# Performance work log

Measured on AMD Instinct MI355X. Metric: run time of the kernel, lower is better.

Reference implementation:

```python
import jax, jax.numpy as jnp
import numpy as np

B, N, F, L = 8, 2048, 128, 2
SLOPE = 0.1  # LeakyReLU negative slope

def lrelu(v):
    return jnp.where(v >= 0, v, SLOPE * v)

def setup_inputs() -> dict:
    key = jax.random.key(0)
    ks = jax.random.split(key, 7)
    scale = 1.0 / np.sqrt(F)
    return {
        "x": jax.random.normal(ks[0], (B, N, F), dtype=jnp.float32),
        "W3": jax.random.normal(ks[1], (L, F, F), dtype=jnp.float32) * scale,
        "b3": jnp.zeros((L, F), dtype=jnp.float32),
        "W4": jax.random.normal(ks[2], (L, F, F), dtype=jnp.float32) * scale,
        "b4": jnp.zeros((L, F), dtype=jnp.float32),
        "W5": jax.random.normal(ks[3], (L, F, F), dtype=jnp.float32) * scale,
        "b5": jnp.zeros((L, F), dtype=jnp.float32),
    }

def reference(x, W3, b3, W4, b4, W5, b5):
    # GraphStack of L GraphLayer modules, mes_type '0':
    #   weight_ij = dot(LeakyReLU(g3(n_i)), LeakyReLU(g4(n_j)))
    #   message_i = mean_{j != i} weight_ij * n_j
    #   n_i_out   = LeakyReLU(g5(message_i)) + n_i
    n = x.shape[1]
    for l in range(W3.shape[0]):
        w1 = lrelu(jnp.einsum('bnf,fg->bng', x, W3[l]) + b3[l])  # [B,N,F]
        w2 = lrelu(jnp.einsum('bnf,fg->bng', x, W4[l]) + b4[l])  # [B,N,F]
        wt = jnp.einsum('bif,bjf->bij', w1, w2)                  # pairwise weights [B,N,N]
        diag = jnp.einsum('bif,bif->bi', w1, w2)                 # self weights to exclude
        msg = (jnp.einsum('bij,bjf->bif', wt, x) - diag[..., None] * x) / (n - 1)
        x = lrelu(jnp.einsum('bif,fg->big', msg, W5[l]) + b5[l]) + x
    return x
```

## Files before the change

kernel.cpp:

```cpp
#include <hip/hip_runtime.h>

#define BB 8
#define NN 2048
#define FF 128
#define NL 2
#define SLOPE 0.1f
#define NROW (BB * NN)
#define XS_STRIDE 136

typedef __attribute__((ext_vector_type(8))) short short8;
typedef __attribute__((ext_vector_type(4))) float f32x4;

__device__ __forceinline__ float lrelu(float v) { return v >= 0.f ? v : SLOPE * v; }

__device__ __forceinline__ ushort f2bf(float f) {
    uint u = __float_as_uint(f);
    return (ushort)((u + 0x7fffu + ((u >> 16) & 1u)) >> 16);
}

__global__ __launch_bounds__(256) void k_prep(
    const float* __restrict__ W3, const float* __restrict__ W4,
    const float* __restrict__ W5, ushort* __restrict__ Wt)
{
    const int idx = blockIdx.x * 256 + threadIdx.x;
    const int m = idx >> 14;
    const int rem = idx & 16383;
    const int f = rem & 127;
    const int g = rem >> 7;
    const int l = m / 3, w = m % 3;
    const float* src = (w == 0) ? W3 : (w == 1) ? W4 : W5;
    Wt[m * 16384 + g * 128 + f] = f2bf(src[l * 16384 + f * 128 + g]);
}

__global__ __launch_bounds__(256) void k_w12(
    const float* __restrict__ x, const ushort* __restrict__ w3t,
    const ushort* __restrict__ w4t, const float* __restrict__ b3,
    const float* __restrict__ b4, ushort* __restrict__ w1b,
    ushort* __restrict__ w2t, ushort* __restrict__ xt,
    float* __restrict__ diag)
{
    __shared__ ushort xs[32 * XS_STRIDE];
    __shared__ float diag_s[32];

    const int tid = threadIdx.x;
    const int row0 = blockIdx.x * 32;
    const int b = row0 >> 11;
    const int jloc0 = row0 & 2047;

    if (tid < 32) diag_s[tid] = 0.f;

    const float4* xg4 = (const float4*)(x + (size_t)row0 * FF);
#pragma unroll
    for (int i = 0; i < 4; i++) {
        const int f4 = i * 256 + tid;
        const int row = f4 >> 5;
        const int k = (f4 & 31) * 4;
        float4 v = xg4[f4];
        ushort4 h;
        h.x = f2bf(v.x); h.y = f2bf(v.y); h.z = f2bf(v.z); h.w = f2bf(v.w);
        *(ushort4*)&xs[row * XS_STRIDE + k] = h;
    }
    __syncthreads();

    {
        const int g = tid >> 1;
        const int h = tid & 1;
        uint p[8];
#pragma unroll
        for (int jj = 0; jj < 8; jj++) {
            const uint lo = xs[(h * 16 + jj * 2) * XS_STRIDE + g];
            const uint hi = xs[(h * 16 + jj * 2 + 1) * XS_STRIDE + g];
            p[jj] = lo | (hi << 16);
        }
        uint4* dst = (uint4*)&xt[(size_t)b * (FF * NN) + (size_t)g * NN + jloc0 + h * 16];
        dst[0] = make_uint4(p[0], p[1], p[2], p[3]);
        dst[1] = make_uint4(p[4], p[5], p[6], p[7]);
    }

    const int lane = tid & 63;
    const int wave = tid >> 6;
    const int c = lane & 15;
    const int quad = lane >> 4;
    const int ct0 = wave * 2;

    f32x4 acc1[2][2], acc2[2][2];
#pragma unroll
    for (int rt = 0; rt < 2; rt++)
#pragma unroll
        for (int ct = 0; ct < 2; ct++) { acc1[rt][ct] = (f32x4)0.f; acc2[rt][ct] = (f32x4)0.f; }

#pragma unroll
    for (int kk = 0; kk < 4; kk++) {
        short8 a0 = *(const short8*)&xs[c * XS_STRIDE + kk * 32 + quad * 8];
        short8 a1 = *(const short8*)&xs[(16 + c) * XS_STRIDE + kk * 32 + quad * 8];
#pragma unroll
        for (int ct = 0; ct < 2; ct++) {
            const int n = (ct0 + ct) * 16 + c;
            short8 bf3 = *(const short8*)&w3t[n * 128 + kk * 32 + quad * 8];
            short8 bf4 = *(const short8*)&w4t[n * 128 + kk * 32 + quad * 8];
            acc1[0][ct] = __builtin_amdgcn_mfma_f32_16x16x32_bf16(a0, bf3, acc1[0][ct], 0, 0, 0);
            acc1[1][ct] = __builtin_amdgcn_mfma_f32_16x16x32_bf16(a1, bf3, acc1[1][ct], 0, 0, 0);
            acc2[0][ct] = __builtin_amdgcn_mfma_f32_16x16x32_bf16(a0, bf4, acc2[0][ct], 0, 0, 0);
            acc2[1][ct] = __builtin_amdgcn_mfma_f32_16x16x32_bf16(a1, bf4, acc2[1][ct], 0, 0, 0);
        }
    }

    float dpar[2][4];
#pragma unroll
    for (int rt = 0; rt < 2; rt++)
#pragma unroll
        for (int r = 0; r < 4; r++) dpar[rt][r] = 0.f;

#pragma unroll
    for (int rt = 0; rt < 2; rt++) {
#pragma unroll
        for (int ct = 0; ct < 2; ct++) {
            const int gcol = (ct0 + ct) * 16 + c;
            const float bb3 = b3[gcol], bb4 = b4[gcol];
            ushort w2p[4];
#pragma unroll
            for (int r = 0; r < 4; r++) {
                const float v1 = lrelu(acc1[rt][ct][r] + bb3);
                const float v2 = lrelu(acc2[rt][ct][r] + bb4);
                const int grow = row0 + rt * 16 + quad * 4 + r;
                w1b[(size_t)grow * FF + gcol] = f2bf(v1);
                w2p[r] = f2bf(v2);
                dpar[rt][r] += v1 * v2;
            }
            const uint lo = (uint)w2p[0] | ((uint)w2p[1] << 16);
            const uint hi = (uint)w2p[2] | ((uint)w2p[3] << 16);
            uint2* dst = (uint2*)&w2t[(size_t)b * (FF * NN) + (size_t)gcol * NN +
                                      jloc0 + rt * 16 + quad * 4];
            *dst = make_uint2(lo, hi);
        }
    }

#pragma unroll
    for (int rt = 0; rt < 2; rt++) {
#pragma unroll
        for (int r = 0; r < 4; r++) {
            float dp = dpar[rt][r];
            dp += __shfl_xor(dp, 1, 64);
            dp += __shfl_xor(dp, 2, 64);
            dp += __shfl_xor(dp, 4, 64);
            dp += __shfl_xor(dp, 8, 64);
            if (c == 0) atomicAdd(&diag_s[rt * 16 + quad * 4 + r], dp);
        }
    }
    __syncthreads();
    if (tid < 32) diag[row0 + tid] = diag_s[tid];
}

__global__ __launch_bounds__(256) void k_S2(
    const ushort* __restrict__ xt, const ushort* __restrict__ w2t,
    ushort* __restrict__ St)
{
    __shared__ float red[4][512];
    const int tid = threadIdx.x;
    const int lane = tid & 63;
    const int wave = tid >> 6;
    const int c = lane & 15;
    const int quad = lane >> 4;

    const int b  = blockIdx.x >> 5;
    const int gq = (blockIdx.x >> 3) & 3;
    const int fs = blockIdx.x & 7;

    const ushort* xtb = xt + (size_t)b * (FF * NN);
    const ushort* w2b = w2t + (size_t)b * (FF * NN);

    const int j0 = wave * 512 + quad * 8;
    const ushort* a0p = &xtb[(gq * 32 + c) * NN + j0];
    const ushort* a1p = &xtb[(gq * 32 + 16 + c) * NN + j0];
    const ushort* bp  = &w2b[(fs * 16 + c) * NN + j0];

    f32x4 acc0 = (f32x4)0.f, acc1 = (f32x4)0.f;
#pragma unroll
    for (int it = 0; it < 16; it++) {
        short8 a0 = *(const short8*)(a0p + it * 32);
        short8 a1 = *(const short8*)(a1p + it * 32);
        short8 bf = *(const short8*)(bp + it * 32);
        acc0 = __builtin_amdgcn_mfma_f32_16x16x32_bf16(a0, bf, acc0, 0, 0, 0);
        acc1 = __builtin_amdgcn_mfma_f32_16x16x32_bf16(a1, bf, acc1, 0, 0, 0);
    }

#pragma unroll
    for (int r = 0; r < 4; r++) {
        red[wave][(quad * 4 + r) * 16 + c] = acc0[r];
        red[wave][(16 + quad * 4 + r) * 16 + c] = acc1[r];
    }
    __syncthreads();

#pragma unroll
    for (int i = 0; i < 2; i++) {
        const int idx = i * 256 + tid;
        const float s = red[0][idx] + red[1][idx] + red[2][idx] + red[3][idx];
        const int gl = idx >> 4;
        const int fl = idx & 15;
        St[(size_t)b * (FF * FF) + (size_t)(gq * 32 + gl) * FF + fs * 16 + fl] = f2bf(s);
    }
}

__global__ __launch_bounds__(256) void k_out(
    const float* __restrict__ x, const ushort* __restrict__ w1b,
    const ushort* __restrict__ St, const float* __restrict__ diag,
    const ushort* __restrict__ w5t, const float* __restrict__ b5,
    float* __restrict__ out)
{
    __shared__ ushort w1s[32 * XS_STRIDE];
    __shared__ ushort ms[32 * XS_STRIDE];

    const int tid = threadIdx.x;
    const int row0 = blockIdx.x * 32;
    const int b = row0 >> 11;
    const ushort* Sb = St + (size_t)b * (FF * FF);

#pragma unroll
    for (int i = 0; i < 2; i++) {
        const int e8 = i * 256 + tid;
        const int off = e8 * 8;
        const int row = off >> 7;
        const int k = off & 127;
        short8 v = *(const short8*)&w1b[(size_t)row0 * FF + off];
        *(short8*)&w1s[row * XS_STRIDE + k] = v;
    }
    __syncthreads();

    const int lane = tid & 63;
    const int wave = tid >> 6;
    const int c = lane & 15;
    const int quad = lane >> 4;
    const int ct0 = wave * 2;

    f32x4 accm[2][2];
#pragma unroll
    for (int rt = 0; rt < 2; rt++)
#pragma unroll
        for (int ct = 0; ct < 2; ct++) accm[rt][ct] = (f32x4)0.f;

#pragma unroll
    for (int kk = 0; kk < 4; kk++) {
        short8 a0 = *(const short8*)&w1s[c * XS_STRIDE + kk * 32 + quad * 8];
        short8 a1 = *(const short8*)&w1s[(16 + c) * XS_STRIDE + kk * 32 + quad * 8];
#pragma unroll
        for (int ct = 0; ct < 2; ct++) {
            const int n = (ct0 + ct) * 16 + c;
            short8 bf = *(const short8*)&Sb[n * 128 + kk * 32 + quad * 8];
            accm[0][ct] = __builtin_amdgcn_mfma_f32_16x16x32_bf16(a0, bf, accm[0][ct], 0, 0, 0);
            accm[1][ct] = __builtin_amdgcn_mfma_f32_16x16x32_bf16(a1, bf, accm[1][ct], 0, 0, 0);
        }
    }

    const float inv = 1.f / (float)(NN - 1);
    float xsv[2][2][4];
#pragma unroll
    for (int rt = 0; rt < 2; rt++) {
        float dg[4];
#pragma unroll
        for (int r = 0; r < 4; r++) dg[r] = diag[row0 + rt * 16 + quad * 4 + r];
#pragma unroll
        for (int ct = 0; ct < 2; ct++) {
            const int gcol = (ct0 + ct) * 16 + c;
#pragma unroll
            for (int r = 0; r < 4; r++) {
                const int lrow = rt * 16 + quad * 4 + r;
                const float xv = x[(size_t)(row0 + lrow) * FF + gcol];
                xsv[rt][ct][r] = xv;
                const float m = (accm[rt][ct][r] - dg[r] * xv) * inv;
                ms[lrow * XS_STRIDE + gcol] = f2bf(m);
            }
        }
    }
    __syncthreads();

    f32x4 acc2[2][2];
#pragma unroll
    for (int rt = 0; rt < 2; rt++)
#pragma unroll
        for (int ct = 0; ct < 2; ct++) acc2[rt][ct] = (f32x4)0.f;

#pragma unroll
    for (int kk = 0; kk < 4; kk++) {
        short8 a0 = *(const short8*)&ms[c * XS_STRIDE + kk * 32 + quad * 8];
        short8 a1 = *(const short8*)&ms[(16 + c) * XS_STRIDE + kk * 32 + quad * 8];
#pragma unroll
        for (int ct = 0; ct < 2; ct++) {
            const int n = (ct0 + ct) * 16 + c;
            short8 bf = *(const short8*)&w5t[n * 128 + kk * 32 + quad * 8];
            acc2[0][ct] = __builtin_amdgcn_mfma_f32_16x16x32_bf16(a0, bf, acc2[0][ct], 0, 0, 0);
            acc2[1][ct] = __builtin_amdgcn_mfma_f32_16x16x32_bf16(a1, bf, acc2[1][ct], 0, 0, 0);
        }
    }

#pragma unroll
    for (int rt = 0; rt < 2; rt++) {
#pragma unroll
        for (int ct = 0; ct < 2; ct++) {
            const int gcol = (ct0 + ct) * 16 + c;
            const float bb = b5[gcol];
#pragma unroll
            for (int r = 0; r < 4; r++) {
                const int grow = row0 + rt * 16 + quad * 4 + r;
                out[(size_t)grow * FF + gcol] = lrelu(acc2[rt][ct][r] + bb) + xsv[rt][ct][r];
            }
        }
    }
}

__global__ __launch_bounds__(256) void k_out_w12(
    const float* __restrict__ x, const ushort* __restrict__ w1b_in,
    const ushort* __restrict__ St, const float* __restrict__ diag_in,
    const ushort* __restrict__ w5t, const float* __restrict__ b5,
    float* __restrict__ out,
    const ushort* __restrict__ w3t, const ushort* __restrict__ w4t,
    const float* __restrict__ b3, const float* __restrict__ b4,
    ushort* __restrict__ w1b, ushort* __restrict__ w2t,
    ushort* __restrict__ xt, float* __restrict__ diag)
{
    __shared__ ushort sA[32 * XS_STRIDE];
    __shared__ ushort sB[32 * XS_STRIDE];
    __shared__ float diag_s[32];

    const int tid = threadIdx.x;
    const int row0 = blockIdx.x * 32;
    const int b = row0 >> 11;
    const int jloc0 = row0 & 2047;
    const ushort* Sb = St + (size_t)b * (FF * FF);

    if (tid < 32) diag_s[tid] = 0.f;

#pragma unroll
    for (int i = 0; i < 2; i++) {
        const int e8 = i * 256 + tid;
        const int off = e8 * 8;
        const int row = off >> 7;
        const int k = off & 127;
        short8 v = *(const short8*)&w1b_in[(size_t)row0 * FF + off];
        *(short8*)&sA[row * XS_STRIDE + k] = v;
    }
    __syncthreads();

    const int lane = tid & 63;
    const int wave = tid >> 6;
    const int c = lane & 15;
    const int quad = lane >> 4;
    const int ct0 = wave * 2;

    f32x4 accm[2][2];
#pragma unroll
    for (int rt = 0; rt < 2; rt++)
#pragma unroll
        for (int ct = 0; ct < 2; ct++) accm[rt][ct] = (f32x4)0.f;

#pragma unroll
    for (int kk = 0; kk < 4; kk++) {
        short8 a0 = *(const short8*)&sA[c * XS_STRIDE + kk * 32 + quad * 8];
        short8 a1 = *(const short8*)&sA[(16 + c) * XS_STRIDE + kk * 32 + quad * 8];
#pragma unroll
        for (int ct = 0; ct < 2; ct++) {
            const int n = (ct0 + ct) * 16 + c;
            short8 bf = *(const short8*)&Sb[n * 128 + kk * 32 + quad * 8];
            accm[0][ct] = __builtin_amdgcn_mfma_f32_16x16x32_bf16(a0, bf, accm[0][ct], 0, 0, 0);
            accm[1][ct] = __builtin_amdgcn_mfma_f32_16x16x32_bf16(a1, bf, accm[1][ct], 0, 0, 0);
        }
    }

    const float inv = 1.f / (float)(NN - 1);
    float xsv[2][2][4];
#pragma unroll
    for (int rt = 0; rt < 2; rt++) {
        float dg[4];
#pragma unroll
        for (int r = 0; r < 4; r++) dg[r] = diag_in[row0 + rt * 16 + quad * 4 + r];
#pragma unroll
        for (int ct = 0; ct < 2; ct++) {
            const int gcol = (ct0 + ct) * 16 + c;
#pragma unroll
            for (int r = 0; r < 4; r++) {
                const int lrow = rt * 16 + quad * 4 + r;
                const float xv = x[(size_t)(row0 + lrow) * FF + gcol];
                xsv[rt][ct][r] = xv;
                const float m = (accm[rt][ct][r] - dg[r] * xv) * inv;
                sB[lrow * XS_STRIDE + gcol] = f2bf(m);
            }
        }
    }
    __syncthreads();

    f32x4 acc2[2][2];
#pragma unroll
    for (int rt = 0; rt < 2; rt++)
#pragma unroll
        for (int ct = 0; ct < 2; ct++) acc2[rt][ct] = (f32x4)0.f;

#pragma unroll
    for (int kk = 0; kk < 4; kk++) {
        short8 a0 = *(const short8*)&sB[c * XS_STRIDE + kk * 32 + quad * 8];
        short8 a1 = *(const short8*)&sB[(16 + c) * XS_STRIDE + kk * 32 + quad * 8];
#pragma unroll
        for (int ct = 0; ct < 2; ct++) {
            const int n = (ct0 + ct) * 16 + c;
            short8 bf = *(const short8*)&w5t[n * 128 + kk * 32 + quad * 8];
            acc2[0][ct] = __builtin_amdgcn_mfma_f32_16x16x32_bf16(a0, bf, acc2[0][ct], 0, 0, 0);
            acc2[1][ct] = __builtin_amdgcn_mfma_f32_16x16x32_bf16(a1, bf, acc2[1][ct], 0, 0, 0);
        }
    }

#pragma unroll
    for (int rt = 0; rt < 2; rt++) {
#pragma unroll
        for (int ct = 0; ct < 2; ct++) {
            const int gcol = (ct0 + ct) * 16 + c;
            const float bb = b5[gcol];
#pragma unroll
            for (int r = 0; r < 4; r++) {
                const int lrow = rt * 16 + quad * 4 + r;
                const float ov = lrelu(acc2[rt][ct][r] + bb) + xsv[rt][ct][r];
                out[(size_t)(row0 + lrow) * FF + gcol] = ov;
                sA[lrow * XS_STRIDE + gcol] = f2bf(ov);
            }
        }
    }
    __syncthreads();

    {
        const int g = tid >> 1;
        const int h = tid & 1;
        uint p[8];
#pragma unroll
        for (int jj = 0; jj < 8; jj++) {
            const uint lo = sA[(h * 16 + jj * 2) * XS_STRIDE + g];
            const uint hi = sA[(h * 16 + jj * 2 + 1) * XS_STRIDE + g];
            p[jj] = lo | (hi << 16);
        }
        uint4* dst = (uint4*)&xt[(size_t)b * (FF * NN) + (size_t)g * NN + jloc0 + h * 16];
        dst[0] = make_uint4(p[0], p[1], p[2], p[3]);
        dst[1] = make_uint4(p[4], p[5], p[6], p[7]);
    }

    f32x4 acc1n[2][2], acc2n[2][2];
#pragma unroll
    for (int rt = 0; rt < 2; rt++)
#pragma unroll
        for (int ct = 0; ct < 2; ct++) { acc1n[rt][ct] = (f32x4)0.f; acc2n[rt][ct] = (f32x4)0.f; }

#pragma unroll
    for (int kk = 0; kk < 4; kk++) {
        short8 a0 = *(const short8*)&sA[c * XS_STRIDE + kk * 32 + quad * 8];
        short8 a1 = *(const short8*)&sA[(16 + c) * XS_STRIDE + kk * 32 + quad * 8];
#pragma unroll
        for (int ct = 0; ct < 2; ct++) {
            const int n = (ct0 + ct) * 16 + c;
            short8 bf3 = *(const short8*)&w3t[n * 128 + kk * 32 + quad * 8];
            short8 bf4 = *(const short8*)&w4t[n * 128 + kk * 32 + quad * 8];
            acc1n[0][ct] = __builtin_amdgcn_mfma_f32_16x16x32_bf16(a0, bf3, acc1n[0][ct], 0, 0, 0);
            acc1n[1][ct] = __builtin_amdgcn_mfma_f32_16x16x32_bf16(a1, bf3, acc1n[1][ct], 0, 0, 0);
            acc2n[0][ct] = __builtin_amdgcn_mfma_f32_16x16x32_bf16(a0, bf4, acc2n[0][ct], 0, 0, 0);
            acc2n[1][ct] = __builtin_amdgcn_mfma_f32_16x16x32_bf16(a1, bf4, acc2n[1][ct], 0, 0, 0);
        }
    }

    float dpar[2][4];
#pragma unroll
    for (int rt = 0; rt < 2; rt++)
#pragma unroll
        for (int r = 0; r < 4; r++) dpar[rt][r] = 0.f;

#pragma unroll
    for (int rt = 0; rt < 2; rt++) {
#pragma unroll
        for (int ct = 0; ct < 2; ct++) {
            const int gcol = (ct0 + ct) * 16 + c;
            const float bb3 = b3[gcol], bb4 = b4[gcol];
            ushort w2p[4];
#pragma unroll
            for (int r = 0; r < 4; r++) {
                const float v1 = lrelu(acc1n[rt][ct][r] + bb3);
                const float v2 = lrelu(acc2n[rt][ct][r] + bb4);
                const int grow = row0 + rt * 16 + quad * 4 + r;
                w1b[(size_t)grow * FF + gcol] = f2bf(v1);
                w2p[r] = f2bf(v2);
                dpar[rt][r] += v1 * v2;
            }
            const uint lo = (uint)w2p[0] | ((uint)w2p[1] << 16);
            const uint hi = (uint)w2p[2] | ((uint)w2p[3] << 16);
            uint2* dst = (uint2*)&w2t[(size_t)b * (FF * NN) + (size_t)gcol * NN +
                                      jloc0 + rt * 16 + quad * 4];
            *dst = make_uint2(lo, hi);
        }
    }

#pragma unroll
    for (int rt = 0; rt < 2; rt++) {
#pragma unroll
        for (int r = 0; r < 4; r++) {
            float dp = dpar[rt][r];
            dp += __shfl_xor(dp, 1, 64);
            dp += __shfl_xor(dp, 2, 64);
            dp += __shfl_xor(dp, 4, 64);
            dp += __shfl_xor(dp, 8, 64);
            if (c == 0) atomicAdd(&diag_s[rt * 16 + quad * 4 + r], dp);
        }
    }
    __syncthreads();
    if (tid < 32) diag[row0 + tid] = diag_s[tid];
}

extern "C" void kernel_launch(void* const* d_in, const int* in_sizes, int n_in,
                              void* d_out, int out_size, void* d_ws, size_t ws_size,
                              hipStream_t stream)
{
    const float* x  = (const float*)d_in[0];
    const float* W3 = (const float*)d_in[1];
    const float* b3 = (const float*)d_in[2];
    const float* W4 = (const float*)d_in[3];
    const float* b4 = (const float*)d_in[4];
    const float* W5 = (const float*)d_in[5];
    const float* b5 = (const float*)d_in[6];
    float* out = (float*)d_out;

    char* ws = (char*)d_ws;
    ushort* w1b   = (ushort*)(ws);
    ushort* w2t   = (ushort*)(ws + ((size_t)4  << 20));
    ushort* xt    = (ushort*)(ws + ((size_t)8  << 20));
    float*  diag  = (float*) (ws + ((size_t)12 << 20));
    ushort* St    = (ushort*)(ws + ((size_t)13 << 20));
    ushort* Wt    = (ushort*)(ws + ((size_t)14 << 20));

    const ushort* w3t0 = Wt;
    const ushort* w4t0 = Wt + 16384;
    const ushort* w5t0 = Wt + 2 * 16384;
    const ushort* w3t1 = Wt + 3 * 16384;
    const ushort* w4t1 = Wt + 4 * 16384;
    const ushort* w5t1 = Wt + 5 * 16384;

    const int rowBlocks = NROW / 32;

    k_prep<<<384, 256, 0, stream>>>(W3, W4, W5, Wt);

    k_w12<<<rowBlocks, 256, 0, stream>>>(x, w3t0, w4t0, b3, b4, w1b, w2t, xt, diag);
    k_S2<<<256, 256, 0, stream>>>(xt, w2t, St);
    k_out_w12<<<rowBlocks, 256, 0, stream>>>(x, w1b, St, diag, w5t0, b5, out,
                                             w3t1, w4t1, b3 + FF, b4 + FF,
                                             w1b, w2t, xt, diag);
    k_S2<<<256, 256, 0, stream>>>(xt, w2t, St);
    k_out<<<rowBlocks, 256, 0, stream>>>(out, w1b, St, diag, w5t1, b5 + FF, out);
}
```

Baseline: 122.9 us.

## Fuse all layers into one cooperative persistent kernel with grid syncs

Replaces the six-kernel launch chain with a single cooperative kernel of 256 blocks, each handling 64 rows. Grid-wide barriers separate the phases. w1 and the diagonal stay in shared memory across phases instead of round-tripping through global memory. This removes launch gaps and some global traffic, but adds five grid.sync barriers and halves the block count, which lowers parallelism in the row phases. The old multi-kernel path is kept as a fallback if the cooperative launch fails.

```diff
diff --git a/kernel.cpp b/kernel.cpp
--- a/kernel.cpp
+++ b/kernel.cpp
@@ -1,11 +1,11 @@
 #include <hip/hip_runtime.h>
-
-#define BB 8
+#include <hip/hip_cooperative_groups.h>
+
+namespace cg = cooperative_groups;
+
 #define NN 2048
 #define FF 128
-#define NL 2
 #define SLOPE 0.1f
-#define NROW (BB * NN)
 #define XS_STRIDE 136
 
 typedef __attribute__((ext_vector_type(8))) short short8;
@@ -17,6 +17,415 @@
     uint u = __float_as_uint(f);
     return (ushort)((u + 0x7fffu + ((u >> 16) & 1u)) >> 16);
 }
+
+
+__device__ __forceinline__ void mfma_AB(
+    const ushort* __restrict__ As, const ushort* __restrict__ Bg,
+    int c, int quad, int ct0, f32x4 acc[2][2])
+{
+#pragma unroll
+    for (int kk = 0; kk < 4; kk++) {
+        short8 a0 = *(const short8*)&As[c * XS_STRIDE + kk * 32 + quad * 8];
+        short8 a1 = *(const short8*)&As[(16 + c) * XS_STRIDE + kk * 32 + quad * 8];
+#pragma unroll
+        for (int ct = 0; ct < 2; ct++) {
+            const int n = (ct0 + ct) * 16 + c;
+            short8 bf = *(const short8*)&Bg[n * 128 + kk * 32 + quad * 8];
+            acc[0][ct] = __builtin_amdgcn_mfma_f32_16x16x32_bf16(a0, bf, acc[0][ct], 0, 0, 0);
+            acc[1][ct] = __builtin_amdgcn_mfma_f32_16x16x32_bf16(a1, bf, acc[1][ct], 0, 0, 0);
+        }
+    }
+}
+
+__device__ __forceinline__ void write_xt32(
+    const ushort* __restrict__ s, ushort* __restrict__ xt,
+    int tid, int b, int jloc0)
+{
+    const int g = tid >> 1;
+    const int h = tid & 1;
+    uint p[8];
+#pragma unroll
+    for (int jj = 0; jj < 8; jj++) {
+        const uint lo = s[(h * 16 + jj * 2) * XS_STRIDE + g];
+        const uint hi = s[(h * 16 + jj * 2 + 1) * XS_STRIDE + g];
+        p[jj] = lo | (hi << 16);
+    }
+    uint4* dst = (uint4*)&xt[(size_t)b * (FF * NN) + (size_t)g * NN + jloc0 + h * 16];
+    dst[0] = make_uint4(p[0], p[1], p[2], p[3]);
+    dst[1] = make_uint4(p[4], p[5], p[6], p[7]);
+}
+
+__device__ __forceinline__ void w12_epilogue32(
+    const f32x4 acc1[2][2], const f32x4 acc2[2][2],
+    const float* __restrict__ b3, const float* __restrict__ b4,
+    ushort* __restrict__ w1dst, ushort* __restrict__ w2t, float* __restrict__ diag_s,
+    int b, int jloc0, int c, int quad, int ct0)
+{
+    float dpar[2][4];
+#pragma unroll
+    for (int rt = 0; rt < 2; rt++)
+#pragma unroll
+        for (int r = 0; r < 4; r++) dpar[rt][r] = 0.f;
+
+#pragma unroll
+    for (int rt = 0; rt < 2; rt++) {
+#pragma unroll
+        for (int ct = 0; ct < 2; ct++) {
+            const int gcol = (ct0 + ct) * 16 + c;
+            const float bb3 = b3[gcol], bb4 = b4[gcol];
+            ushort w2p[4];
+#pragma unroll
+            for (int r = 0; r < 4; r++) {
+                const float v1 = lrelu(acc1[rt][ct][r] + bb3);
+                const float v2 = lrelu(acc2[rt][ct][r] + bb4);
+                const int lrow = rt * 16 + quad * 4 + r;
+                w1dst[lrow * XS_STRIDE + gcol] = f2bf(v1);
+                w2p[r] = f2bf(v2);
+                dpar[rt][r] += v1 * v2;
+            }
+            const uint lo = (uint)w2p[0] | ((uint)w2p[1] << 16);
+            const uint hi = (uint)w2p[2] | ((uint)w2p[3] << 16);
+            *(uint2*)&w2t[(size_t)b * (FF * NN) + (size_t)gcol * NN +
+                          jloc0 + rt * 16 + quad * 4] = make_uint2(lo, hi);
+        }
+    }
+#pragma unroll
+    for (int rt = 0; rt < 2; rt++) {
+#pragma unroll
+        for (int r = 0; r < 4; r++) {
+            float dp = dpar[rt][r];
+            dp += __shfl_xor(dp, 1, 64);
+            dp += __shfl_xor(dp, 2, 64);
+            dp += __shfl_xor(dp, 4, 64);
+            dp += __shfl_xor(dp, 8, 64);
+            if (c == 0) atomicAdd(&diag_s[rt * 16 + quad * 4 + r], dp);
+        }
+    }
+}
+
+__device__ __forceinline__ void s_phase256(
+    const ushort* __restrict__ xt, const ushort* __restrict__ w2t,
+    ushort* __restrict__ St, float (*red)[512],
+    int blk, int tid, int wave, int c, int quad)
+{
+    const int sb = blk >> 5;
+    const int gq = (blk >> 3) & 3;
+    const int fs = blk & 7;
+
+    const int j0 = wave * 512 + quad * 8;
+    const ushort* a0p = &xt[(size_t)sb * (FF * NN) + (size_t)(gq * 32 + c) * NN + j0];
+    const ushort* a1p = &xt[(size_t)sb * (FF * NN) + (size_t)(gq * 32 + 16 + c) * NN + j0];
+    const ushort* bp  = &w2t[(size_t)sb * (FF * NN) + (size_t)(fs * 16 + c) * NN + j0];
+
+    f32x4 acc0 = (f32x4)0.f, acc1 = (f32x4)0.f;
+#pragma unroll
+    for (int it = 0; it < 16; it++) {
+        short8 a0 = *(const short8*)(a0p + it * 32);
+        short8 a1 = *(const short8*)(a1p + it * 32);
+        short8 bf = *(const short8*)(bp + it * 32);
+        acc0 = __builtin_amdgcn_mfma_f32_16x16x32_bf16(a0, bf, acc0, 0, 0, 0);
+        acc1 = __builtin_amdgcn_mfma_f32_16x16x32_bf16(a1, bf, acc1, 0, 0, 0);
+    }
+#pragma unroll
+    for (int r = 0; r < 4; r++) {
+        red[wave][(quad * 4 + r) * 16 + c] = acc0[r];
+        red[wave][(16 + quad * 4 + r) * 16 + c] = acc1[r];
+    }
+    __syncthreads();
+#pragma unroll
+    for (int i = 0; i < 2; i++) {
+        const int idx = i * 256 + tid;
+        const float s = red[0][idx] + red[1][idx] + red[2][idx] + red[3][idx];
+        const int gl = idx >> 4, fl = idx & 15;
+        St[(size_t)sb * (FF * FF) + (size_t)(gq * 32 + gl) * FF + fs * 16 + fl] = f2bf(s);
+    }
+}
+
+
+__device__ __forceinline__ void mfma_AB64(
+    const ushort* __restrict__ As, const ushort* __restrict__ Bg,
+    int c, int quad, int ct0, f32x4 acc[4][2])
+{
+#pragma unroll
+    for (int kk = 0; kk < 4; kk++) {
+        short8 a[4];
+#pragma unroll
+        for (int rt = 0; rt < 4; rt++)
+            a[rt] = *(const short8*)&As[(rt * 16 + c) * XS_STRIDE + kk * 32 + quad * 8];
+#pragma unroll
+        for (int ct = 0; ct < 2; ct++) {
+            const int n = (ct0 + ct) * 16 + c;
+            short8 bf = *(const short8*)&Bg[n * 128 + kk * 32 + quad * 8];
+#pragma unroll
+            for (int rt = 0; rt < 4; rt++)
+                acc[rt][ct] = __builtin_amdgcn_mfma_f32_16x16x32_bf16(a[rt], bf, acc[rt][ct], 0, 0, 0);
+        }
+    }
+}
+
+__device__ __forceinline__ void write_xt64(
+    const ushort* __restrict__ s, ushort* __restrict__ xt,
+    int tid, int b, int jloc0)
+{
+    const int g = tid >> 1;
+    const int h = tid & 1;
+    uint p[16];
+#pragma unroll
+    for (int jj = 0; jj < 16; jj++) {
+        const uint lo = s[(h * 32 + jj * 2) * XS_STRIDE + g];
+        const uint hi = s[(h * 32 + jj * 2 + 1) * XS_STRIDE + g];
+        p[jj] = lo | (hi << 16);
+    }
+    uint4* dst = (uint4*)&xt[(size_t)b * (FF * NN) + (size_t)g * NN + jloc0 + h * 32];
+    dst[0] = make_uint4(p[0], p[1], p[2], p[3]);
+    dst[1] = make_uint4(p[4], p[5], p[6], p[7]);
+    dst[2] = make_uint4(p[8], p[9], p[10], p[11]);
+    dst[3] = make_uint4(p[12], p[13], p[14], p[15]);
+}
+
+__device__ __forceinline__ void w12_epilogue64(
+    const f32x4 acc1[4][2], const f32x4 acc2[4][2],
+    const float* __restrict__ b3, const float* __restrict__ b4,
+    ushort* __restrict__ w1dst, ushort* __restrict__ w2t, float* __restrict__ diag_s,
+    int b, int jloc0, int c, int quad, int ct0)
+{
+    float dpar[4][4];
+#pragma unroll
+    for (int rt = 0; rt < 4; rt++)
+#pragma unroll
+        for (int r = 0; r < 4; r++) dpar[rt][r] = 0.f;
+
+#pragma unroll
+    for (int rt = 0; rt < 4; rt++) {
+#pragma unroll
+        for (int ct = 0; ct < 2; ct++) {
+            const int gcol = (ct0 + ct) * 16 + c;
+            const float bb3 = b3[gcol], bb4 = b4[gcol];
+            ushort w2p[4];
+#pragma unroll
+            for (int r = 0; r < 4; r++) {
+                const float v1 = lrelu(acc1[rt][ct][r] + bb3);
+                const float v2 = lrelu(acc2[rt][ct][r] + bb4);
+                const int lrow = rt * 16 + quad * 4 + r;
+                w1dst[lrow * XS_STRIDE + gcol] = f2bf(v1);
+                w2p[r] = f2bf(v2);
+                dpar[rt][r] += v1 * v2;
+            }
+            const uint lo = (uint)w2p[0] | ((uint)w2p[1] << 16);
+            const uint hi = (uint)w2p[2] | ((uint)w2p[3] << 16);
+            *(uint2*)&w2t[(size_t)b * (FF * NN) + (size_t)gcol * NN +
+                          jloc0 + rt * 16 + quad * 4] = make_uint2(lo, hi);
+        }
+    }
+#pragma unroll
+    for (int rt = 0; rt < 4; rt++) {
+#pragma unroll
+        for (int r = 0; r < 4; r++) {
+            float dp = dpar[rt][r];
+            dp += __shfl_xor(dp, 1, 64);
+            dp += __shfl_xor(dp, 2, 64);
+            dp += __shfl_xor(dp, 4, 64);
+            dp += __shfl_xor(dp, 8, 64);
+            if (c == 0) atomicAdd(&diag_s[rt * 16 + quad * 4 + r], dp);
+        }
+    }
+}
+
+__global__ __launch_bounds__(256, 2) void k_all(
+    const float* __restrict__ x,
+    const float* __restrict__ W3, const float* __restrict__ b3,
+    const float* __restrict__ W4, const float* __restrict__ b4,
+    const float* __restrict__ W5, const float* __restrict__ b5,
+    float* __restrict__ out,
+    ushort* __restrict__ w2t, ushort* __restrict__ xt,
+    ushort* __restrict__ St, ushort* __restrict__ Wt)
+{
+    cg::grid_group grid = cg::this_grid();
+
+    __shared__ ushort sW[64 * XS_STRIDE];
+    __shared__ ushort sT[64 * XS_STRIDE];
+    __shared__ float red[4][512];
+    __shared__ float diag_s[64];
+
+    const int tid = threadIdx.x;
+    const int blk = blockIdx.x;
+    const int lane = tid & 63;
+    const int wave = tid >> 6;
+    const int c = lane & 15;
+    const int quad = lane >> 4;
+    const int ct0 = wave * 2;
+
+    const int row0 = blk * 64;
+    const int b = blk >> 5;
+    const int jloc0 = row0 & 2047;
+    const float inv = 1.f / (float)(NN - 1);
+
+    for (int idx = blk * 256 + tid; idx < 6 * 16384; idx += 65536) {
+        const int rem = idx & 16383;
+        const int f = rem & 127, g = rem >> 7;
+        const int m = idx >> 14;
+        const int l = m / 3, w = m % 3;
+        const float* src = (w == 0) ? W3 : (w == 1) ? W4 : W5;
+        Wt[idx] = f2bf(src[l * 16384 + f * 128 + g]);
+    }
+
+    if (tid < 64) diag_s[tid] = 0.f;
+
+    {
+        const float4* xg4 = (const float4*)(x + (size_t)row0 * FF);
+#pragma unroll
+        for (int i = 0; i < 8; i++) {
+            const int f4 = i * 256 + tid;
+            const int row = f4 >> 5;
+            const int k = (f4 & 31) * 4;
+            float4 v = xg4[f4];
+            ushort4 h;
+            h.x = f2bf(v.x); h.y = f2bf(v.y); h.z = f2bf(v.z); h.w = f2bf(v.w);
+            *(ushort4*)&sT[row * XS_STRIDE + k] = h;
+        }
+    }
+
+    __threadfence(); grid.sync(); __threadfence();
+
+    write_xt64(sT, xt, tid, b, jloc0);
+    {
+        f32x4 a1[4][2], a2[4][2];
+#pragma unroll
+        for (int rt = 0; rt < 4; rt++)
+#pragma unroll
+            for (int ct = 0; ct < 2; ct++) { a1[rt][ct] = (f32x4)0.f; a2[rt][ct] = (f32x4)0.f; }
+        mfma_AB64(sT, Wt, c, quad, ct0, a1);
+        mfma_AB64(sT, Wt + 16384, c, quad, ct0, a2);
+        w12_epilogue64(a1, a2, b3, b4, sW, w2t, diag_s, b, jloc0, c, quad, ct0);
+    }
+
+    __threadfence(); grid.sync(); __threadfence();
+
+    s_phase256(xt, w2t, St, red, blk, tid, wave, c, quad);
+
+    __threadfence(); grid.sync(); __threadfence();
+
+    {
+        const ushort* Sb = St + (size_t)b * (FF * FF);
+        f32x4 accm[4][2];
+#pragma unroll
+        for (int rt = 0; rt < 4; rt++)
+#pragma unroll
+            for (int ct = 0; ct < 2; ct++) accm[rt][ct] = (f32x4)0.f;
+        mfma_AB64(sW, Sb, c, quad, ct0, accm);
+
+#pragma unroll
+        for (int rt = 0; rt < 4; rt++) {
+            float dg[4];
+#pragma unroll
+            for (int r = 0; r < 4; r++) dg[r] = diag_s[rt * 16 + quad * 4 + r];
+#pragma unroll
+            for (int ct = 0; ct < 2; ct++) {
+                const int gcol = (ct0 + ct) * 16 + c;
+#pragma unroll
+                for (int r = 0; r < 4; r++) {
+                    const int lrow = rt * 16 + quad * 4 + r;
+                    const float xv = x[(size_t)(row0 + lrow) * FF + gcol];
+                    sT[lrow * XS_STRIDE + gcol] = f2bf((accm[rt][ct][r] - dg[r] * xv) * inv);
+                }
+            }
+        }
+        __syncthreads();
+        if (tid < 64) diag_s[tid] = 0.f;
+
+        f32x4 acc2[4][2];
+#pragma unroll
+        for (int rt = 0; rt < 4; rt++)
+#pragma unroll
+            for (int ct = 0; ct < 2; ct++) acc2[rt][ct] = (f32x4)0.f;
+        mfma_AB64(sT, Wt + 2 * 16384, c, quad, ct0, acc2);
+
+#pragma unroll
+        for (int rt = 0; rt < 4; rt++) {
+#pragma unroll
+            for (int ct = 0; ct < 2; ct++) {
+                const int gcol = (ct0 + ct) * 16 + c;
+                const float bb = b5[gcol];
+#pragma unroll
+                for (int r = 0; r < 4; r++) {
+                    const int lrow = rt * 16 + quad * 4 + r;
+                    const float ov = lrelu(acc2[rt][ct][r] + bb) +
+                                     x[(size_t)(row0 + lrow) * FF + gcol];
+                    out[(size_t)(row0 + lrow) * FF + gcol] = ov;
+                    sW[lrow * XS_STRIDE + gcol] = f2bf(ov);
+                }
+            }
+        }
+        __syncthreads();
+
+        write_xt64(sW, xt, tid, b, jloc0);
+        f32x4 a1[4][2], a2[4][2];
+#pragma unroll
+        for (int rt = 0; rt < 4; rt++)
+#pragma unroll
+            for (int ct = 0; ct < 2; ct++) { a1[rt][ct] = (f32x4)0.f; a2[rt][ct] = (f32x4)0.f; }
+        mfma_AB64(sW, Wt + 3 * 16384, c, quad, ct0, a1);
+        mfma_AB64(sW, Wt + 4 * 16384, c, quad, ct0, a2);
+        w12_epilogue64(a1, a2, b3 + FF, b4 + FF, sT, w2t, diag_s, b, jloc0, c, quad, ct0);
+    }
+
+    __threadfence(); grid.sync(); __threadfence();
+
+    s_phase256(xt, w2t, St, red, blk, tid, wave, c, quad);
+
+    __threadfence(); grid.sync(); __threadfence();
+
+    {
+        const ushort* Sb = St + (size_t)b * (FF * FF);
+        f32x4 accm[4][2];
+#pragma unroll
+        for (int rt = 0; rt < 4; rt++)
+#pragma unroll
+            for (int ct = 0; ct < 2; ct++) accm[rt][ct] = (f32x4)0.f;
+        mfma_AB64(sT, Sb, c, quad, ct0, accm);
+
+#pragma unroll
+        for (int rt = 0; rt < 4; rt++) {
+            float dg[4];
+#pragma unroll
+            for (int r = 0; r < 4; r++) dg[r] = diag_s[rt * 16 + quad * 4 + r];
+#pragma unroll
+            for (int ct = 0; ct < 2; ct++) {
+                const int gcol = (ct0 + ct) * 16 + c;
+#pragma unroll
+                for (int r = 0; r < 4; r++) {
+                    const int lrow = rt * 16 + quad * 4 + r;
+                    const float xv = out[(size_t)(row0 + lrow) * FF + gcol];
+                    sW[lrow * XS_STRIDE + gcol] = f2bf((accm[rt][ct][r] - dg[r] * xv) * inv);
+                }
+            }
+        }
+        __syncthreads();
+
+        f32x4 acc2[4][2];
+#pragma unroll
+        for (int rt = 0; rt < 4; rt++)
+#pragma unroll
+            for (int ct = 0; ct < 2; ct++) acc2[rt][ct] = (f32x4)0.f;
+        mfma_AB64(sW, Wt + 5 * 16384, c, quad, ct0, acc2);
+
+#pragma unroll
+        for (int rt = 0; rt < 4; rt++) {
+#pragma unroll
+            for (int ct = 0; ct < 2; ct++) {
+                const int gcol = (ct0 + ct) * 16 + c;
+                const float bb = b5[FF + gcol];
+#pragma unroll
+                for (int r = 0; r < 4; r++) {
+                    const int lrow = rt * 16 + quad * 4 + r;
+                    const size_t oidx = (size_t)(row0 + lrow) * FF + gcol;
+                    out[oidx] = lrelu(acc2[rt][ct][r] + bb) + out[oidx];
+                }
+            }
+        }
+    }
+}
+
 
 __global__ __launch_bounds__(256) void k_prep(
     const float* __restrict__ W3, const float* __restrict__ W4,
@@ -62,20 +471,7 @@
     }
     __syncthreads();
 
-    {
-        const int g = tid >> 1;
-        const int h = tid & 1;
-        uint p[8];
-#pragma unroll
-        for (int jj = 0; jj < 8; jj++) {
-            const uint lo = xs[(h * 16 + jj * 2) * XS_STRIDE + g];
-            const uint hi = xs[(h * 16 + jj * 2 + 1) * XS_STRIDE + g];
-            p[jj] = lo | (hi << 16);
-        }
-        uint4* dst = (uint4*)&xt[(size_t)b * (FF * NN) + (size_t)g * NN + jloc0 + h * 16];
-        dst[0] = make_uint4(p[0], p[1], p[2], p[3]);
-        dst[1] = make_uint4(p[4], p[5], p[6], p[7]);
-    }
+    write_xt32(xs, xt, tid, b, jloc0);
 
     const int lane = tid & 63;
     const int wave = tid >> 6;
@@ -83,34 +479,19 @@
     const int quad = lane >> 4;
     const int ct0 = wave * 2;
 
-    f32x4 acc1[2][2], acc2[2][2];
+    f32x4 a1[2][2], a2[2][2];
 #pragma unroll
     for (int rt = 0; rt < 2; rt++)
 #pragma unroll
-        for (int ct = 0; ct < 2; ct++) { acc1[rt][ct] = (f32x4)0.f; acc2[rt][ct] = (f32x4)0.f; }
-
-#pragma unroll
-    for (int kk = 0; kk < 4; kk++) {
-        short8 a0 = *(const short8*)&xs[c * XS_STRIDE + kk * 32 + quad * 8];
-        short8 a1 = *(const short8*)&xs[(16 + c) * XS_STRIDE + kk * 32 + quad * 8];
-#pragma unroll
-        for (int ct = 0; ct < 2; ct++) {
-            const int n = (ct0 + ct) * 16 + c;
-            short8 bf3 = *(const short8*)&w3t[n * 128 + kk * 32 + quad * 8];
-            short8 bf4 = *(const short8*)&w4t[n * 128 + kk * 32 + quad * 8];
-            acc1[0][ct] = __builtin_amdgcn_mfma_f32_16x16x32_bf16(a0, bf3, acc1[0][ct], 0, 0, 0);
-            acc1[1][ct] = __builtin_amdgcn_mfma_f32_16x16x32_bf16(a1, bf3, acc1[1][ct], 0, 0, 0);
-            acc2[0][ct] = __builtin_amdgcn_mfma_f32_16x16x32_bf16(a0, bf4, acc2[0][ct], 0, 0, 0);
-            acc2[1][ct] = __builtin_amdgcn_mfma_f32_16x16x32_bf16(a1, bf4, acc2[1][ct], 0, 0, 0);
-        }
-    }
+        for (int ct = 0; ct < 2; ct++) { a1[rt][ct] = (f32x4)0.f; a2[rt][ct] = (f32x4)0.f; }
+    mfma_AB(xs, w3t, c, quad, ct0, a1);
+    mfma_AB(xs, w4t, c, quad, ct0, a2);
 
     float dpar[2][4];
 #pragma unroll
     for (int rt = 0; rt < 2; rt++)
 #pragma unroll
         for (int r = 0; r < 4; r++) dpar[rt][r] = 0.f;
-
 #pragma unroll
     for (int rt = 0; rt < 2; rt++) {
 #pragma unroll
@@ -120,8 +501,8 @@
             ushort w2p[4];
 #pragma unroll
             for (int r = 0; r < 4; r++) {
-                const float v1 = lrelu(acc1[rt][ct][r] + bb3);
-                const float v2 = lrelu(acc2[rt][ct][r] + bb4);
+                const float v1 = lrelu(a1[rt][ct][r] + bb3);
+                const float v2 = lrelu(a2[rt][ct][r] + bb4);
                 const int grow = row0 + rt * 16 + quad * 4 + r;
                 w1b[(size_t)grow * FF + gcol] = f2bf(v1);
                 w2p[r] = f2bf(v2);
@@ -129,12 +510,10 @@
             }
             const uint lo = (uint)w2p[0] | ((uint)w2p[1] << 16);
             const uint hi = (uint)w2p[2] | ((uint)w2p[3] << 16);
-            uint2* dst = (uint2*)&w2t[(size_t)b * (FF * NN) + (size_t)gcol * NN +
-                                      jloc0 + rt * 16 + quad * 4];
-            *dst = make_uint2(lo, hi);
-        }
-    }
-
+            *(uint2*)&w2t[(size_t)b * (FF * NN) + (size_t)gcol * NN +
+                          jloc0 + rt * 16 + quad * 4] = make_uint2(lo, hi);
+        }
+    }
 #pragma unroll
     for (int rt = 0; rt < 2; rt++) {
 #pragma unroll
@@ -157,48 +536,10 @@
 {
     __shared__ float red[4][512];
     const int tid = threadIdx.x;
-    const int lane = tid & 63;
     const int wave = tid >> 6;
-    const int c = lane & 15;
-    const int quad = lane >> 4;
-
-    const int b  = blockIdx.x >> 5;
-    const int gq = (blockIdx.x >> 3) & 3;
-    const int fs = blockIdx.x & 7;
-
-    const ushort* xtb = xt + (size_t)b * (FF * NN);
-    const ushort* w2b = w2t + (size_t)b * (FF * NN);
-
-    const int j0 = wave * 512 + quad * 8;
-    const ushort* a0p = &xtb[(gq * 32 + c) * NN + j0];
-    const ushort* a1p = &xtb[(gq * 32 + 16 + c) * NN + j0];
-    const ushort* bp  = &w2b[(fs * 16 + c) * NN + j0];
-
-    f32x4 acc0 = (f32x4)0.f, acc1 = (f32x4)0.f;
-#pragma unroll
-    for (int it = 0; it < 16; it++) {
-        short8 a0 = *(const short8*)(a0p + it * 32);
-        short8 a1 = *(const short8*)(a1p + it * 32);
-        short8 bf = *(const short8*)(bp + it * 32);
-        acc0 = __builtin_amdgcn_mfma_f32_16x16x32_bf16(a0, bf, acc0, 0, 0, 0);
-        acc1 = __builtin_amdgcn_mfma_f32_16x16x32_bf16(a1, bf, acc1, 0, 0, 0);
-    }
-
-#pragma unroll
-    for (int r = 0; r < 4; r++) {
-        red[wave][(quad * 4 + r) * 16 + c] = acc0[r];
-        red[wave][(16 + quad * 4 + r) * 16 + c] = acc1[r];
-    }
-    __syncthreads();
-
-#pragma unroll
-    for (int i = 0; i < 2; i++) {
-        const int idx = i * 256 + tid;
-        const float s = red[0][idx] + red[1][idx] + red[2][idx] + red[3][idx];
-        const int gl = idx >> 4;
-        const int fl = idx & 15;
-        St[(size_t)b * (FF * FF) + (size_t)(gq * 32 + gl) * FF + fs * 16 + fl] = f2bf(s);
-    }
+    const int c = tid & 15;
+    const int quad = (tid & 63) >> 4;
+    s_phase256(xt, w2t, St, red, blockIdx.x, tid, wave, c, quad);
 }
 
 __global__ __launch_bounds__(256) void k_out(
@@ -217,12 +558,10 @@
 
 #pragma unroll
     for (int i = 0; i < 2; i++) {
-        const int e8 = i * 256 + tid;
-        const int off = e8 * 8;
+        const int off = (i * 256 + tid) * 8;
         const int row = off >> 7;
         const int k = off & 127;
-        short8 v = *(const short8*)&w1b[(size_t)row0 * FF + off];
-        *(short8*)&w1s[row * XS_STRIDE + k] = v;
+        *(short8*)&w1s[row * XS_STRIDE + k] = *(const short8*)&w1b[(size_t)row0 * FF + off];
     }
     __syncthreads();
 
@@ -237,19 +576,7 @@
     for (int rt = 0; rt < 2; rt++)
 #pragma unroll
         for (int ct = 0; ct < 2; ct++) accm[rt][ct] = (f32x4)0.f;
-
-#pragma unroll
-    for (int kk = 0; kk < 4; kk++) {
-        short8 a0 = *(const short8*)&w1s[c * XS_STRIDE + kk * 32 + quad * 8];
-        short8 a1 = *(const short8*)&w1s[(16 + c) * XS_STRIDE + kk * 32 + quad * 8];
-#pragma unroll
-        for (int ct = 0; ct < 2; ct++) {
-            const int n = (ct0 + ct) * 16 + c;
-            short8 bf = *(const short8*)&Sb[n * 128 + kk * 32 + quad * 8];
-            accm[0][ct] = __builtin_amdgcn_mfma_f32_16x16x32_bf16(a0, bf, accm[0][ct], 0, 0, 0);
-            accm[1][ct] = __builtin_amdgcn_mfma_f32_16x16x32_bf16(a1, bf, accm[1][ct], 0, 0, 0);
-        }
-    }
+    mfma_AB(w1s, Sb, c, quad, ct0, accm);
 
     const float inv = 1.f / (float)(NN - 1);
     float xsv[2][2][4];
@@ -266,8 +593,7 @@
                 const int lrow = rt * 16 + quad * 4 + r;
                 const float xv = x[(size_t)(row0 + lrow) * FF + gcol];
                 xsv[rt][ct][r] = xv;
-                const float m = (accm[rt][ct][r] - dg[r] * xv) * inv;
-                ms[lrow * XS_STRIDE + gcol] = f2bf(m);
+                ms[lrow * XS_STRIDE + gcol] = f2bf((accm[rt][ct][r] - dg[r] * xv) * inv);
             }
         }
     }
@@ -278,19 +604,7 @@
     for (int rt = 0; rt < 2; rt++)
 #pragma unroll
         for (int ct = 0; ct < 2; ct++) acc2[rt][ct] = (f32x4)0.f;
-
-#pragma unroll
-    for (int kk = 0; kk < 4; kk++) {
-        short8 a0 = *(const short8*)&ms[c * XS_STRIDE + kk * 32 + quad * 8];
-        short8 a1 = *(const short8*)&ms[(16 + c) * XS_STRIDE + kk * 32 + quad * 8];
-#pragma unroll
-        for (int ct = 0; ct < 2; ct++) {
-            const int n = (ct0 + ct) * 16 + c;
-            short8 bf = *(const short8*)&w5t[n * 128 + kk * 32 + quad * 8];
-            acc2[0][ct] = __builtin_amdgcn_mfma_f32_16x16x32_bf16(a0, bf, acc2[0][ct], 0, 0, 0);
-            acc2[1][ct] = __builtin_amdgcn_mfma_f32_16x16x32_bf16(a1, bf, acc2[1][ct], 0, 0, 0);
-        }
-    }
+    mfma_AB(ms, w5t, c, quad, ct0, acc2);
 
 #pragma unroll
     for (int rt = 0; rt < 2; rt++) {
@@ -331,12 +645,10 @@
 
 #pragma unroll
     for (int i = 0; i < 2; i++) {
-        const int e8 = i * 256 + tid;
-        const int off = e8 * 8;
+        const int off = (i * 256 + tid) * 8;
         const int row = off >> 7;
         const int k = off & 127;
-        short8 v = *(const short8*)&w1b_in[(size_t)row0 * FF + off];
-        *(short8*)&sA[row * XS_STRIDE + k] = v;
+        *(short8*)&sA[row * XS_STRIDE + k] = *(const short8*)&w1b_in[(size_t)row0 * FF + off];
     }
     __syncthreads();
 
@@ -351,19 +663,7 @@
     for (int rt = 0; rt < 2; rt++)
 #pragma unroll
         for (int ct = 0; ct < 2; ct++) accm[rt][ct] = (f32x4)0.f;
-
-#pragma unroll
-    for (int kk = 0; kk < 4; kk++) {
-        short8 a0 = *(const short8*)&sA[c * XS_STRIDE + kk * 32 + quad * 8];
-        short8 a1 = *(const short8*)&sA[(16 + c) * XS_STRIDE + kk * 32 + quad * 8];
-#pragma unroll
-        for (int ct = 0; ct < 2; ct++) {
-            const int n = (ct0 + ct) * 16 + c;
-            short8 bf = *(const short8*)&Sb[n * 128 + kk * 32 + quad * 8];
-            accm[0][ct] = __builtin_amdgcn_mfma_f32_16x16x32_bf16(a0, bf, accm[0][ct], 0, 0, 0);
-            accm[1][ct] = __builtin_amdgcn_mfma_f32_16x16x32_bf16(a1, bf, accm[1][ct], 0, 0, 0);
-        }
-    }
+    mfma_AB(sA, Sb, c, quad, ct0, accm);
 
     const float inv = 1.f / (float)(NN - 1);
     float xsv[2][2][4];
@@ -380,8 +680,7 @@
                 const int lrow = rt * 16 + quad * 4 + r;
                 const float xv = x[(size_t)(row0 + lrow) * FF + gcol];
                 xsv[rt][ct][r] = xv;
-                const float m = (accm[rt][ct][r] - dg[r] * xv) * inv;
-                sB[lrow * XS_STRIDE + gcol] = f2bf(m);
+                sB[lrow * XS_STRIDE + gcol] = f2bf((accm[rt][ct][r] - dg[r] * xv) * inv);
             }
         }
     }
@@ -392,19 +691,7 @@
     for (int rt = 0; rt < 2; rt++)
 #pragma unroll
         for (int ct = 0; ct < 2; ct++) acc2[rt][ct] = (f32x4)0.f;
-
-#pragma unroll
-    for (int kk = 0; kk < 4; kk++) {
-        short8 a0 = *(const short8*)&sB[c * XS_STRIDE + kk * 32 + quad * 8];
-        short8 a1 = *(const short8*)&sB[(16 + c) * XS_STRIDE + kk * 32 + quad * 8];
-#pragma unroll
-        for (int ct = 0; ct < 2; ct++) {
-            const int n = (ct0 + ct) * 16 + c;
-            short8 bf = *(const short8*)&w5t[n * 128 + kk * 32 + quad * 8];
-            acc2[0][ct] = __builtin_amdgcn_mfma_f32_16x16x32_bf16(a0, bf, acc2[0][ct], 0, 0, 0);
-            acc2[1][ct] = __builtin_amdgcn_mfma_f32_16x16x32_bf16(a1, bf, acc2[1][ct], 0, 0, 0);
-        }
-    }
+    mfma_AB(sB, w5t, c, quad, ct0, acc2);
 
 #pragma unroll
     for (int rt = 0; rt < 2; rt++) {
@@ -423,49 +710,20 @@
     }
     __syncthreads();
 
-    {
-        const int g = tid >> 1;
-        const int h = tid & 1;
-        uint p[8];
-#pragma unroll
-        for (int jj = 0; jj < 8; jj++) {
-            const uint lo = sA[(h * 16 + jj * 2) * XS_STRIDE + g];
-            const uint hi = sA[(h * 16 + jj * 2 + 1) * XS_STRIDE + g];
-            p[jj] = lo | (hi << 16);
-        }
-        uint4* dst = (uint4*)&xt[(size_t)b * (FF * NN) + (size_t)g * NN + jloc0 + h * 16];
-        dst[0] = make_uint4(p[0], p[1], p[2], p[3]);
-        dst[1] = make_uint4(p[4], p[5], p[6], p[7]);
-    }
-
-    f32x4 acc1n[2][2], acc2n[2][2];
+    write_xt32(sA, xt, tid, b, jloc0);
+    f32x4 a1[2][2], a2[2][2];
 #pragma unroll
     for (int rt = 0; rt < 2; rt++)
 #pragma unroll
-        for (int ct = 0; ct < 2; ct++) { acc1n[rt][ct] = (f32x4)0.f; acc2n[rt][ct] = (f32x4)0.f; }
-
-#pragma unroll
-    for (int kk = 0; kk < 4; kk++) {
-        short8 a0 = *(const short8*)&sA[c * XS_STRIDE + kk * 32 + quad * 8];
-        short8 a1 = *(const short8*)&sA[(16 + c) * XS_STRIDE + kk * 32 + quad * 8];
-#pragma unroll
-        for (int ct = 0; ct < 2; ct++) {
-            const int n = (ct0 + ct) * 16 + c;
-            short8 bf3 = *(const short8*)&w3t[n * 128 + kk * 32 + quad * 8];
-            short8 bf4 = *(const short8*)&w4t[n * 128 + kk * 32 + quad * 8];
-            acc1n[0][ct] = __builtin_amdgcn_mfma_f32_16x16x32_bf16(a0, bf3, acc1n[0][ct], 0, 0, 0);
-            acc1n[1][ct] = __builtin_amdgcn_mfma_f32_16x16x32_bf16(a1, bf3, acc1n[1][ct], 0, 0, 0);
-            acc2n[0][ct] = __builtin_amdgcn_mfma_f32_16x16x32_bf16(a0, bf4, acc2n[0][ct], 0, 0, 0);
-            acc2n[1][ct] = __builtin_amdgcn_mfma_f32_16x16x32_bf16(a1, bf4, acc2n[1][ct], 0, 0, 0);
-        }
-    }
+        for (int ct = 0; ct < 2; ct++) { a1[rt][ct] = (f32x4)0.f; a2[rt][ct] = (f32x4)0.f; }
+    mfma_AB(sA, w3t, c, quad, ct0, a1);
+    mfma_AB(sA, w4t, c, quad, ct0, a2);
 
     float dpar[2][4];
 #pragma unroll
     for (int rt = 0; rt < 2; rt++)
 #pragma unroll
         for (int r = 0; r < 4; r++) dpar[rt][r] = 0.f;
-
 #pragma unroll
     for (int rt = 0; rt < 2; rt++) {
 #pragma unroll
@@ -475,8 +733,8 @@
             ushort w2p[4];
 #pragma unroll
             for (int r = 0; r < 4; r++) {
-                const float v1 = lrelu(acc1n[rt][ct][r] + bb3);
-                const float v2 = lrelu(acc2n[rt][ct][r] + bb4);
+                const float v1 = lrelu(a1[rt][ct][r] + bb3);
+                const float v2 = lrelu(a2[rt][ct][r] + bb4);
                 const int grow = row0 + rt * 16 + quad * 4 + r;
                 w1b[(size_t)grow * FF + gcol] = f2bf(v1);
                 w2p[r] = f2bf(v2);
@@ -484,12 +742,10 @@
             }
             const uint lo = (uint)w2p[0] | ((uint)w2p[1] << 16);
             const uint hi = (uint)w2p[2] | ((uint)w2p[3] << 16);
-            uint2* dst = (uint2*)&w2t[(size_t)b * (FF * NN) + (size_t)gcol * NN +
-                                      jloc0 + rt * 16 + quad * 4];
-            *dst = make_uint2(lo, hi);
-        }
-    }
-
+            *(uint2*)&w2t[(size_t)b * (FF * NN) + (size_t)gcol * NN +
+                          jloc0 + rt * 16 + quad * 4] = make_uint2(lo, hi);
+        }
+    }
 #pragma unroll
     for (int rt = 0; rt < 2; rt++) {
 #pragma unroll
@@ -520,29 +776,29 @@
     float* out = (float*)d_out;
 
     char* ws = (char*)d_ws;
-    ushort* w1b   = (ushort*)(ws);
-    ushort* w2t   = (ushort*)(ws + ((size_t)4  << 20));
-    ushort* xt    = (ushort*)(ws + ((size_t)8  << 20));
-    float*  diag  = (float*) (ws + ((size_t)12 << 20));
-    ushort* St    = (ushort*)(ws + ((size_t)13 << 20));
-    ushort* Wt    = (ushort*)(ws + ((size_t)14 << 20));
-
-    const ushort* w3t0 = Wt;
-    const ushort* w4t0 = Wt + 16384;
-    const ushort* w5t0 = Wt + 2 * 16384;
-    const ushort* w3t1 = Wt + 3 * 16384;
-    const ushort* w4t1 = Wt + 4 * 16384;
-    const ushort* w5t1 = Wt + 5 * 16384;
-
-    const int rowBlocks = NROW / 32;
-
-    k_prep<<<384, 256, 0, stream>>>(W3, W4, W5, Wt);
-
-    k_w12<<<rowBlocks, 256, 0, stream>>>(x, w3t0, w4t0, b3, b4, w1b, w2t, xt, diag);
-    k_S2<<<256, 256, 0, stream>>>(xt, w2t, St);
-    k_out_w12<<<rowBlocks, 256, 0, stream>>>(x, w1b, St, diag, w5t0, b5, out,
-                                             w3t1, w4t1, b3 + FF, b4 + FF,
-                                             w1b, w2t, xt, diag);
-    k_S2<<<256, 256, 0, stream>>>(xt, w2t, St);
-    k_out<<<rowBlocks, 256, 0, stream>>>(out, w1b, St, diag, w5t1, b5 + FF, out);
-}
+    ushort* w1b  = (ushort*)(ws);
+    ushort* w2t  = (ushort*)(ws + ((size_t)4  << 20));
+    ushort* xt   = (ushort*)(ws + ((size_t)8  << 20));
+    float*  diag = (float*) (ws + ((size_t)12 << 20));
+    ushort* St   = (ushort*)(ws + ((size_t)13 << 20));
+    ushort* Wt   = (ushort*)(ws + ((size_t)13 << 20) + (512 << 10));
+
+    void* args[] = {
+        (void*)&x, (void*)&W3, (void*)&b3, (void*)&W4, (void*)&b4,
+        (void*)&W5, (void*)&b5, (void*)&out, (void*)&w2t, (void*)&xt,
+        (void*)&St, (void*)&Wt
+    };
+    hipError_t e = hipLaunchCooperativeKernel((void*)k_all, dim3(256), dim3(256),
+                                              args, 0, stream);
+    if (e != hipSuccess) {
+        (void)hipGetLastError();
+        k_prep<<<384, 256, 0, stream>>>(W3, W4, W5, Wt);
+        k_w12<<<512, 256, 0, stream>>>(x, Wt, Wt + 16384, b3, b4, w1b, w2t, xt, diag);
+        k_S2<<<256, 256, 0, stream>>>(xt, w2t, St);
+        k_out_w12<<<512, 256, 0, stream>>>(x, w1b, St, diag, Wt + 2 * 16384, b5, out,
+                                           Wt + 3 * 16384, Wt + 4 * 16384,
+                                           b3 + FF, b4 + FF, w1b, w2t, xt, diag);
+        k_S2<<<256, 256, 0, stream>>>(xt, w2t, St);
+        k_out<<<512, 256, 0, stream>>>(out, w1b, St, diag, Wt + 5 * 16384, b5 + FF, out);
+    }
+}
```

Result: slower. 448.5 us (+265.0%).
